# Kernel optimization log

Hardware: AMD Instinct MI355X
Metric: run time of the kernel (lower is better)

The kernel has to match this reference:

```python
import jax, jax.numpy as jnp
import numpy as np

HEADS = 4
DIM_HEAD = 32
HIDDEN = HEADS * DIM_HEAD  # 128
SCALE = 10.0
EPS = 1e-12  # F.normalize eps


def _l2norm_lastdim(t):
    # F.normalize(t, dim=-1): t / max(||t||_2, eps) along last axis
    n = jnp.sqrt(jnp.sum(t * t, axis=-1, keepdims=True))
    return t / jnp.maximum(n, EPS)


def setup_inputs() -> dict:
    key = jax.random.key(0)
    k1, k2, k3 = jax.random.split(key, 3)
    x = jax.random.normal(k1, (2, 256, 4096), dtype=jnp.float32)
    w_qkv = jax.random.normal(k2, (3 * HIDDEN, 256), dtype=jnp.float32) * 0.05
    w_out = jax.random.normal(k3, (256, HIDDEN), dtype=jnp.float32) * 0.05
    b_out = jnp.zeros((256,), dtype=jnp.float32)
    return {"x": x, "w_qkv": w_qkv, "w_out": w_out, "b_out": b_out}


def reference(x, w_qkv, w_out, b_out):
    b, c, l = x.shape
    # pointwise Conv1d == channel matmul: (3*hidden, c) @ (b, c, l)
    qkv = jnp.einsum('oc,bcl->bol', w_qkv, x)
    q, k, v = jnp.split(qkv, 3, axis=1)
    resh = lambda t: t.reshape(b, HEADS, DIM_HEAD, l)  # (b,h,d,l)
    q, k, v = resh(q), resh(k), resh(v)
    # faithful: normalize over the LAST dim (sequence axis l)
    q = _l2norm_lastdim(q)
    k = _l2norm_lastdim(k)
    sim = jnp.einsum('bhdi,bhdj->bhij', q, k) * SCALE  # (b,h,l,l)
    attn = jax.nn.softmax(sim, axis=-1)
    out = jnp.einsum('bhij,bhdj->bhid', attn, v)  # (b,h,l,d)
    # faithful raw view: row-major reshape of (b,h,l,d) -> (b, h*d, l)
    out = out.reshape(b, HIDDEN, l)
    return jnp.einsum('oc,bcl->bol', w_out, out) + b_out[None, :, None]
```

## Files before the change

kernel.cpp:

```cpp
#include <hip/hip_runtime.h>
#include <math.h>

#define LSEQ 4096
#define CIN  256
#define HID  128
#define O3   384
#define NSP  4
#define JTPS (64 / NSP)

typedef float f32x4 __attribute__((ext_vector_type(4)));
typedef short s16x8 __attribute__((ext_vector_type(8)));
typedef short s16x4 __attribute__((ext_vector_type(4)));

typedef const __attribute__((address_space(1))) char* gp_t;
typedef __attribute__((address_space(3))) char* lp_t;

__device__ __forceinline__ short f2bf(float f) {
    union { float f; unsigned u; } c; c.f = f;
    unsigned r = (c.u + 0x7FFFu + ((c.u >> 16) & 1u)) >> 16;
    return (short)r;
}

__device__ __forceinline__ unsigned cvt_pk_bf16(float lo, float hi) {
    unsigned r;
    asm("v_cvt_pk_bf16_f32 %0, %1, %2" : "=v"(r) : "v"(lo), "v"(hi));
    return r;
}

__device__ __forceinline__ float exp2_hw(float x) {
    float r;
    asm("v_exp_f32 %0, %1" : "=v"(r) : "v"(x));
    return r;
}

__device__ __forceinline__ float bfbits(unsigned v, int hi) {
    union { unsigned u; float f; } c;
    c.u = hi ? (v & 0xffff0000u) : (v << 16);
    return c.f;
}

__global__ __launch_bounds__(256) void pack_xw(const float* __restrict__ x,
                                               const float* __restrict__ wq,
                                               const float* __restrict__ wo,
                                               short* __restrict__ xP,
                                               short* __restrict__ wP,
                                               short* __restrict__ wP2) {
    const int tid = threadIdx.x;
    if (blockIdx.x >= 1024) {
        const int gid = (blockIdx.x - 1024) * 256 + tid;
        s16x8 o;
        if (gid < 12288) {
            const int m = gid & 15, g = (gid >> 4) & 3, ct = (gid >> 6) & 7;
            const int ot = gid >> 9;
            const float* src = wq + (ot * 16 + m) * 256 + ct * 32 + g * 8;
#pragma unroll
            for (int e = 0; e < 8; ++e) o[e] = f2bf(src[e]);
            *(s16x8*)(wP + (size_t)gid * 8) = o;
        } else {
            const int g2 = gid - 12288;
            const int m = g2 & 15, g = (g2 >> 4) & 3, ct = (g2 >> 6) & 3;
            const int ot = g2 >> 8;
            const float* src = wo + (ot * 16 + m) * 128 + ct * 32 + g * 8;
#pragma unroll
            for (int e = 0; e < 8; ++e) o[e] = f2bf(src[e]);
            *(s16x8*)(wP2 + (size_t)g2 * 8) = o;
        }
        return;
    }
    __shared__ float tile[32][68];
    const int b = blockIdx.x >> 9, ct = (blockIdx.x >> 6) & 7, lt = blockIdx.x & 63;
    const int c = tid >> 3, l8 = (tid & 7) * 8;
    const float* xb = x + ((size_t)b * CIN + ct * 32 + c) * LSEQ + lt * 64 + l8;
    *(float4*)&tile[c][l8]     = *(const float4*)xb;
    *(float4*)&tile[c][l8 + 4] = *(const float4*)(xb + 4);
    __syncthreads();
    const int g = tid >> 6, l = tid & 63;
    s16x8 o;
#pragma unroll
    for (int e = 0; e < 8; ++e) o[e] = f2bf(tile[g * 8 + e][l]);
    *(s16x8*)(xP + ((size_t)((b * 8 + ct) * 4 + g) * LSEQ + lt * 64 + l) * 8) = o;
}

__global__ __launch_bounds__(256) void mfma_qkv(const short* __restrict__ xP,
                                                const short* __restrict__ wP,
                                                float* __restrict__ qkv) {
    const int i = blockIdx.x;
    const int slice = i & 31, ot = i >> 5;
    const int b = slice >> 4, lq = slice & 15;
    const int tid = threadIdx.x, lane = tid & 63, w = tid >> 6;
    const int m = lane & 15, g = lane >> 4;
    const int l0 = lq * 256 + w * 64;

    s16x8 wA[8];
#pragma unroll
    for (int ct = 0; ct < 8; ++ct)
        wA[ct] = *(const s16x8*)(wP + ((size_t)((ot * 8 + ct) * 4 + g) * 16 + m) * 8);

    f32x4 acc[4];
#pragma unroll
    for (int t = 0; t < 4; ++t) acc[t] = (f32x4){0.f, 0.f, 0.f, 0.f};

#pragma unroll
    for (int ct = 0; ct < 8; ++ct) {
        const size_t bb = (size_t)((b * 8 + ct) * 4 + g) * LSEQ;
#pragma unroll
        for (int t = 0; t < 4; ++t) {
            const s16x8 xf = *(const s16x8*)(xP + (bb + l0 + t * 16 + m) * 8);
            acc[t] = __builtin_amdgcn_mfma_f32_16x16x32_bf16(wA[ct], xf, acc[t], 0, 0, 0);
        }
    }
    float* qb = qkv + ((size_t)b * O3 + ot * 16) * LSEQ;
#pragma unroll
    for (int t = 0; t < 4; ++t)
#pragma unroll
        for (int r = 0; r < 4; ++r)
            qb[(size_t)(4 * g + r) * LSEQ + l0 + t * 16 + m] = acc[t][r];
}

__global__ __launch_bounds__(256) void k_norm(const float* __restrict__ qkv,
                                              float* __restrict__ scales) {
    const int row = blockIdx.x;
    const int b = row >> 8, o = row & 255;
    const float* p = qkv + ((size_t)b * O3 + o) * LSEQ;
    const int tid = threadIdx.x;
    float ss = 0.f;
#pragma unroll
    for (int r = 0; r < 4; ++r) {
        const float4 v = *(const float4*)(p + (r * 256 + tid) * 4);
        ss += v.x * v.x + v.y * v.y + v.z * v.z + v.w * v.w;
    }
#pragma unroll
    for (int off = 32; off >= 1; off >>= 1) ss += __shfl_xor(ss, off);
    __shared__ float red[4];
    if ((tid & 63) == 0) red[tid >> 6] = ss;
    __syncthreads();
    if (tid == 0) {
        const float tot = red[0] + red[1] + red[2] + red[3];
        const float num = (o < HID) ? 14.4269504088896340736f : 1.0f;
        scales[row] = num / fmaxf(sqrtf(tot), 1e-12f);
    }
}

__global__ __launch_bounds__(256) void k_pack(const float* __restrict__ qkv,
                                              const float* __restrict__ scales,
                                              short* __restrict__ qT,
                                              short* __restrict__ kP,
                                              short* __restrict__ vP) {
    __shared__ float tile[32][68];
    const int tid = threadIdx.x;
    const int bh = blockIdx.x & 7, ch = blockIdx.x >> 3;
    const int b = bh >> 2, h = bh & 3;
    const int l0 = ch * 64;
    const float* qg = qkv + ((size_t)b * O3 + h * 32) * LSEQ;
    const float* kg = qg + (size_t)HID * LSEQ;
    const float* vg = qg + (size_t)2 * HID * LSEQ;
    const size_t bho = (size_t)bh * (LSEQ * 32);
    const int d = tid >> 3, c8 = (tid & 7) * 8;

    *(float4*)&tile[d][c8]     = *(const float4*)(qg + (size_t)d * LSEQ + l0 + c8);
    *(float4*)&tile[d][c8 + 4] = *(const float4*)(qg + (size_t)d * LSEQ + l0 + c8 + 4);
    __syncthreads();
    {
        const int i = tid >> 2, dseg = (tid & 3) * 8;
        const float4 sa = *(const float4*)(scales + b * 256 + h * 32 + dseg);
        const float4 sb = *(const float4*)(scales + b * 256 + h * 32 + dseg + 4);
        const float sc[8] = {sa.x, sa.y, sa.z, sa.w, sb.x, sb.y, sb.z, sb.w};
        s16x8 o;
#pragma unroll
        for (int e = 0; e < 8; ++e) o[e] = f2bf(tile[dseg + e][i] * sc[e]);
        *(s16x8*)(qT + bho + (size_t)(l0 + i) * 32 + dseg) = o;
    }
    __syncthreads();
    *(float4*)&tile[d][c8]     = *(const float4*)(kg + (size_t)d * LSEQ + l0 + c8);
    *(float4*)&tile[d][c8 + 4] = *(const float4*)(kg + (size_t)d * LSEQ + l0 + c8 + 4);
    __syncthreads();
    {
        const int gg = tid >> 6, jl = tid & 63;
        const float4 sa = *(const float4*)(scales + b * 256 + 128 + h * 32 + gg * 8);
        const float4 sb = *(const float4*)(scales + b * 256 + 128 + h * 32 + gg * 8 + 4);
        const float sc[8] = {sa.x, sa.y, sa.z, sa.w, sb.x, sb.y, sb.z, sb.w};
        s16x8 o;
#pragma unroll
        for (int e = 0; e < 8; ++e) o[e] = f2bf(tile[gg * 8 + e][jl] * sc[e]);
        *(s16x8*)(kP + bho + (size_t)ch * 2048 + gg * 512 + jl * 8) = o;
    }
    __syncthreads();
    *(float4*)&tile[d][c8]     = *(const float4*)(vg + (size_t)d * LSEQ + l0 + c8);
    *(float4*)&tile[d][c8 + 4] = *(const float4*)(vg + (size_t)d * LSEQ + l0 + c8 + 4);
    __syncthreads();
    {
        const int s = tid >> 4, dd = (tid & 15) * 2;
        s16x8 o;
#pragma unroll
        for (int u = 0; u < 4; ++u) {
            o[u]     = f2bf(tile[dd][s * 4 + u]);
            o[4 + u] = f2bf(tile[dd + 1][s * 4 + u]);
        }
        *(s16x8*)(vP + bho + (size_t)ch * 2048 + s * 128 + dd * 4) = o;
    }
}

__global__ __launch_bounds__(512, 8) void k_attn(const short* __restrict__ qT,
                                                 const short* __restrict__ kP,
                                                 const short* __restrict__ vP,
                                                 unsigned* __restrict__ pacc2,
                                                 float* __restrict__ plsum) {
    __shared__ float4 lds_v[1024];
    char* lds = (char*)lds_v;
    const int tid = threadIdx.x;
    const int lane = tid & 63, w = tid >> 6;
    const int m = lane & 15, g = lane >> 4;
    const int bh = blockIdx.x & 7;
    const int rest = blockIdx.x >> 3;
    const int iblk = rest & 31, sp = rest >> 5;
    const size_t bho = (size_t)bh * (LSEQ * 32);
    const int i0 = iblk * 128 + w * 16;

    const s16x8 qf = *(const s16x8*)(qT + bho + (size_t)(i0 + m) * 32 + g * 8);
    const char* kPb = (const char*)(kP + bho);
    const char* vPb = (const char*)(vP + bho);

    float lsum = 0.f;
    f32x4 acc0 = {0.f, 0.f, 0.f, 0.f}, acc1 = {0.f, 0.f, 0.f, 0.f};
    const f32x4 zeroc = {0.f, 0.f, 0.f, 0.f};
    const int jt0 = sp * JTPS;

    auto stage = [&](int buf, int jt) {
        const char* src = (tid < 256 ? kPb : vPb) + (size_t)jt * 4096 + (tid & 255) * 16;
        char* dst = lds + buf * 8192 + (tid < 256 ? 0 : 4096) + (w & 3) * 1024;
        __builtin_amdgcn_global_load_lds((gp_t)src, (lp_t)dst, 16, 0, 0);
    };

    stage(0, jt0);
    __syncthreads();

    for (int t = 0; t < JTPS; ++t) {
        const int buf = t & 1;
        if (t + 1 < JTPS) stage(buf ^ 1, jt0 + t + 1);
        const char* kb = lds + buf * 8192;
        const char* vb = kb + 4096;

        f32x4 st[4];
#pragma unroll
        for (int t2 = 0; t2 < 4; ++t2) {
            const s16x8 kf = *(const s16x8*)(kb + g * 1024 + (t2 * 16 + m) * 16);
            st[t2] = __builtin_amdgcn_mfma_f32_16x16x32_bf16(kf, qf, zeroc, 0, 0, 0);
        }

        float p[16];
        float ts0 = 0.f, ts1 = 0.f, ts2 = 0.f, ts3 = 0.f;
#pragma unroll
        for (int t2 = 0; t2 < 4; ++t2) {
            const float e0 = exp2_hw(st[t2][0]);
            const float e1 = exp2_hw(st[t2][1]);
            const float e2 = exp2_hw(st[t2][2]);
            const float e3 = exp2_hw(st[t2][3]);
            p[t2 * 4 + 0] = e0; p[t2 * 4 + 1] = e1;
            p[t2 * 4 + 2] = e2; p[t2 * 4 + 3] = e3;
            ts0 += e0; ts1 += e1; ts2 += e2; ts3 += e3;
        }
        lsum += (ts0 + ts1) + (ts2 + ts3);

        union { unsigned u[4]; s16x8 v; } a0u, a1u;
#pragma unroll
        for (int e = 0; e < 4; ++e) {
            a0u.u[e] = cvt_pk_bf16(p[2 * e],     p[2 * e + 1]);
            a1u.u[e] = cvt_pk_bf16(p[8 + 2 * e], p[9 + 2 * e]);
        }

#pragma unroll
        for (int pp = 0; pp < 2; ++pp) {
            const s16x8 pa = pp ? a1u.v : a0u.v;
#pragma unroll
            for (int n0 = 0; n0 < 2; ++n0) {
                const s16x4 v0 = *(const s16x4*)(vb + (pp * 8 + 0 + g) * 256 + (n0 * 16 + m) * 8);
                const s16x4 v1 = *(const s16x4*)(vb + (pp * 8 + 4 + g) * 256 + (n0 * 16 + m) * 8);
                s16x8 vf;
#pragma unroll
                for (int u = 0; u < 4; ++u) { vf[u] = v0[u]; vf[4 + u] = v1[u]; }
                if (n0 == 0) acc0 = __builtin_amdgcn_mfma_f32_16x16x32_bf16(pa, vf, acc0, 0, 0, 0);
                else         acc1 = __builtin_amdgcn_mfma_f32_16x16x32_bf16(pa, vf, acc1, 0, 0, 0);
            }
        }
        __syncthreads();
    }

    lsum += __shfl_xor(lsum, 16);
    lsum += __shfl_xor(lsum, 32);

    const int pb = (bh * 32 + iblk) * NSP + sp;
    if (g == 0) plsum[(size_t)pb * 128 + w * 16 + m] = lsum;
    unsigned* pa = pacc2 + ((size_t)pb * 128 + w * 16) * 16;
#pragma unroll
    for (int r = 0; r < 4; ++r)
        pa[(g * 4 + r) * 16 + m] = cvt_pk_bf16(acc0[r], acc1[r]);
}

__global__ __launch_bounds__(256) void k_comb(const unsigned* __restrict__ pacc2,
                                              const float* __restrict__ plsum,
                                              short* __restrict__ rawP) {
    const int b = blockIdx.x >> 6, lblk = blockIdx.x & 63;
    const int l0 = lblk * 64;
    const int t = threadIdx.x;
    const int ct2 = t >> 6, g = (t >> 4) & 3, lsub = t & 15;
    const int ii = (l0 + lsub * 4) >> 5;
    const int mm0 = (lsub * 4) & 15;
    const int hi = (lsub >> 2) & 1;

#pragma unroll
    for (int e = 0; e < 8; ++e) {
        const int row0 = (((b * 4 + ct2) * 32) + g * 8 + e) * NSP;
        float ls = 0.f, a0 = 0.f, a1 = 0.f, a2 = 0.f, a3 = 0.f;
#pragma unroll
        for (int sp = 0; sp < NSP; ++sp) {
            const unsigned* pr = pacc2 + ((size_t)(row0 + sp) * 128 + ii) * 16 + mm0;
            const uint4 u = *(const uint4*)pr;
            a0 += bfbits(u.x, hi); a1 += bfbits(u.y, hi);
            a2 += bfbits(u.z, hi); a3 += bfbits(u.w, hi);
            ls += plsum[(size_t)(row0 + sp) * 128 + ii];
        }
        const float inv = 1.0f / ls;
        short* dst = rawP + (((size_t)((b * 4 + ct2) * 4 + g) * LSEQ) + l0 + lsub * 4) * 8 + e;
        dst[0]  = f2bf(a0 * inv);
        dst[8]  = f2bf(a1 * inv);
        dst[16] = f2bf(a2 * inv);
        dst[24] = f2bf(a3 * inv);
    }
}

__global__ __launch_bounds__(256) void mfma_proj(const short* __restrict__ rawP,
                                                 const short* __restrict__ wP2,
                                                 const float* __restrict__ bias,
                                                 float* __restrict__ out) {
    const int i = blockIdx.x;
    const int slice = i & 31, ot = i >> 5;
    const int b = slice >> 4, lq = slice & 15;
    const int tid = threadIdx.x, lane = tid & 63, w = tid >> 6;
    const int m = lane & 15, g = lane >> 4;
    const int l0 = lq * 256 + w * 64;

    s16x8 wA[4];
#pragma unroll
    for (int ct = 0; ct < 4; ++ct)
        wA[ct] = *(const s16x8*)(wP2 + ((size_t)((ot * 4 + ct) * 4 + g) * 16 + m) * 8);

    f32x4 acc[4];
#pragma unroll
    for (int t = 0; t < 4; ++t) acc[t] = (f32x4){0.f, 0.f, 0.f, 0.f};

#pragma unroll
    for (int ct = 0; ct < 4; ++ct) {
        const size_t bb = (size_t)((b * 4 + ct) * 4 + g) * LSEQ;
#pragma unroll
        for (int t = 0; t < 4; ++t) {
            const s16x8 xf = *(const s16x8*)(rawP + (bb + l0 + t * 16 + m) * 8);
            acc[t] = __builtin_amdgcn_mfma_f32_16x16x32_bf16(wA[ct], xf, acc[t], 0, 0, 0);
        }
    }
    float bv[4];
#pragma unroll
    for (int r = 0; r < 4; ++r) bv[r] = bias[ot * 16 + 4 * g + r];
    float* ob = out + ((size_t)b * CIN + ot * 16) * LSEQ;
#pragma unroll
    for (int t = 0; t < 4; ++t)
#pragma unroll
        for (int r = 0; r < 4; ++r)
            ob[(size_t)(4 * g + r) * LSEQ + l0 + t * 16 + m] = acc[t][r] + bv[r];
}

extern "C" void kernel_launch(void* const* d_in, const int* in_sizes, int n_in,
                              void* d_out, int out_size, void* d_ws, size_t ws_size,
                              hipStream_t stream) {
    const float* x     = (const float*)d_in[0];
    const float* w_qkv = (const float*)d_in[1];
    const float* w_out = (const float*)d_in[2];
    const float* b_out = (const float*)d_in[3];
    float* out = (float*)d_out;
    float* ws  = (float*)d_ws;

    float*    qkv    = ws;
    unsigned* pacc2  = (unsigned*)ws;
    short*    rawP   = (short*)(ws + 2097152);
    float*    plsum  = ws + 2621440;
    short*    xP     = (short*)(ws + 3145728);
    short*    qT     = (short*)(ws + 3145728);
    short*    kP     = (short*)(ws + 3670016);
    short*    vP     = (short*)(ws + 4194304);
    short*    wP     = (short*)(ws + 4718592);
    short*    wP2    = (short*)(ws + 4767744);
    float*    scales = ws + 4784128;

    pack_xw  <<<1088, 256, 0, stream>>>(x, w_qkv, w_out, xP, wP, wP2);
    mfma_qkv <<<768,  256, 0, stream>>>(xP, wP, qkv);
    k_norm   <<<512,  256, 0, stream>>>(qkv, scales);
    k_pack   <<<512,  256, 0, stream>>>(qkv, scales, qT, kP, vP);
    k_attn   <<<1024, 512, 0, stream>>>(qT, kP, vP, pacc2, plsum);
    k_comb   <<<128,  256, 0, stream>>>(pacc2, plsum, rawP);
    mfma_proj<<<512,  256, 0, stream>>>(rawP, wP2, b_out, out);
}
```

Baseline: 72.74 us.

## Fuse L2-norm reduction into QKV GEMM, store QKV as bf16, repack V

After: 67.17 us. 7.7% less time.

```diff
diff --git a/kernel.cpp b/kernel.cpp
--- a/kernel.cpp
+++ b/kernel.cpp
@@ -21,6 +21,12 @@
     return (short)r;
 }
 
+__device__ __forceinline__ float bf2f(short s) {
+    union { unsigned u; float f; } c;
+    c.u = ((unsigned)(unsigned short)s) << 16;
+    return c.f;
+}
+
 __device__ __forceinline__ unsigned cvt_pk_bf16(float lo, float hi) {
     unsigned r;
     asm("v_cvt_pk_bf16_f32 %0, %1, %2" : "=v"(r) : "v"(lo), "v"(hi));
@@ -44,9 +50,11 @@
                                                const float* __restrict__ wo,
                                                short* __restrict__ xP,
                                                short* __restrict__ wP,
-                                               short* __restrict__ wP2) {
+                                               short* __restrict__ wP2,
+                                               float* __restrict__ ss) {
     const int tid = threadIdx.x;
     if (blockIdx.x >= 1024) {
+        if (blockIdx.x == 1024) { ss[tid] = 0.f; ss[256 + tid] = 0.f; }
         const int gid = (blockIdx.x - 1024) * 256 + tid;
         s16x8 o;
         if (gid < 12288) {
@@ -83,7 +91,8 @@
 
 __global__ __launch_bounds__(256) void mfma_qkv(const short* __restrict__ xP,
                                                 const short* __restrict__ wP,
-                                                float* __restrict__ qkv) {
+                                                short* __restrict__ qkv,
+                                                float* __restrict__ ss) {
     const int i = blockIdx.x;
     const int slice = i & 31, ot = i >> 5;
     const int b = slice >> 4, lq = slice & 15;
@@ -109,40 +118,34 @@
             acc[t] = __builtin_amdgcn_mfma_f32_16x16x32_bf16(wA[ct], xf, acc[t], 0, 0, 0);
         }
     }
-    float* qb = qkv + ((size_t)b * O3 + ot * 16) * LSEQ;
+    short* qb = qkv + ((size_t)b * O3 + ot * 16) * LSEQ;
 #pragma unroll
     for (int t = 0; t < 4; ++t)
 #pragma unroll
         for (int r = 0; r < 4; ++r)
-            qb[(size_t)(4 * g + r) * LSEQ + l0 + t * 16 + m] = acc[t][r];
-}
-
-__global__ __launch_bounds__(256) void k_norm(const float* __restrict__ qkv,
-                                              float* __restrict__ scales) {
-    const int row = blockIdx.x;
-    const int b = row >> 8, o = row & 255;
-    const float* p = qkv + ((size_t)b * O3 + o) * LSEQ;
-    const int tid = threadIdx.x;
-    float ss = 0.f;
-#pragma unroll
-    for (int r = 0; r < 4; ++r) {
-        const float4 v = *(const float4*)(p + (r * 256 + tid) * 4);
-        ss += v.x * v.x + v.y * v.y + v.z * v.z + v.w * v.w;
-    }
-#pragma unroll
-    for (int off = 32; off >= 1; off >>= 1) ss += __shfl_xor(ss, off);
-    __shared__ float red[4];
-    if ((tid & 63) == 0) red[tid >> 6] = ss;
-    __syncthreads();
-    if (tid == 0) {
-        const float tot = red[0] + red[1] + red[2] + red[3];
-        const float num = (o < HID) ? 14.4269504088896340736f : 1.0f;
-        scales[row] = num / fmaxf(sqrtf(tot), 1e-12f);
-    }
-}
-
-__global__ __launch_bounds__(256) void k_pack(const float* __restrict__ qkv,
-                                              const float* __restrict__ scales,
+            qb[(size_t)(4 * g + r) * LSEQ + l0 + t * 16 + m] = f2bf(acc[t][r]);
+
+    if (ot < 16) {
+        float s4[4];
+#pragma unroll
+        for (int r = 0; r < 4; ++r) {
+            float s = acc[0][r] * acc[0][r];
+#pragma unroll
+            for (int t = 1; t < 4; ++t) s = fmaf(acc[t][r], acc[t][r], s);
+#pragma unroll
+            for (int mk = 1; mk < 16; mk <<= 1) s += __shfl_xor(s, mk);
+            s4[r] = s;
+        }
+        if (m == 0) {
+#pragma unroll
+            for (int r = 0; r < 4; ++r)
+                atomicAdd(ss + b * 256 + ot * 16 + 4 * g + r, s4[r]);
+        }
+    }
+}
+
+__global__ __launch_bounds__(256) void k_pack(const short* __restrict__ qkv,
+                                              const float* __restrict__ ss,
                                               short* __restrict__ qT,
                                               short* __restrict__ kP,
                                               short* __restrict__ vP) {
@@ -151,52 +154,61 @@
     const int bh = blockIdx.x & 7, ch = blockIdx.x >> 3;
     const int b = bh >> 2, h = bh & 3;
     const int l0 = ch * 64;
-    const float* qg = qkv + ((size_t)b * O3 + h * 32) * LSEQ;
-    const float* kg = qg + (size_t)HID * LSEQ;
-    const float* vg = qg + (size_t)2 * HID * LSEQ;
+    const short* qg = qkv + ((size_t)b * O3 + h * 32) * LSEQ;
+    const short* kg = qg + (size_t)HID * LSEQ;
+    const short* vg = qg + (size_t)2 * HID * LSEQ;
     const size_t bho = (size_t)bh * (LSEQ * 32);
     const int d = tid >> 3, c8 = (tid & 7) * 8;
 
-    *(float4*)&tile[d][c8]     = *(const float4*)(qg + (size_t)d * LSEQ + l0 + c8);
-    *(float4*)&tile[d][c8 + 4] = *(const float4*)(qg + (size_t)d * LSEQ + l0 + c8 + 4);
+    {
+        const s16x8 qv = *(const s16x8*)(qg + (size_t)d * LSEQ + l0 + c8);
+#pragma unroll
+        for (int e = 0; e < 8; ++e) tile[d][c8 + e] = bf2f(qv[e]);
+    }
     __syncthreads();
     {
         const int i = tid >> 2, dseg = (tid & 3) * 8;
-        const float4 sa = *(const float4*)(scales + b * 256 + h * 32 + dseg);
-        const float4 sb = *(const float4*)(scales + b * 256 + h * 32 + dseg + 4);
-        const float sc[8] = {sa.x, sa.y, sa.z, sa.w, sb.x, sb.y, sb.z, sb.w};
         s16x8 o;
 #pragma unroll
-        for (int e = 0; e < 8; ++e) o[e] = f2bf(tile[dseg + e][i] * sc[e]);
+        for (int e = 0; e < 8; ++e) {
+            const float sc = 14.4269504088896340736f /
+                             fmaxf(sqrtf(ss[b * 256 + h * 32 + dseg + e]), 1e-12f);
+            o[e] = f2bf(tile[dseg + e][i] * sc);
+        }
         *(s16x8*)(qT + bho + (size_t)(l0 + i) * 32 + dseg) = o;
     }
     __syncthreads();
-    *(float4*)&tile[d][c8]     = *(const float4*)(kg + (size_t)d * LSEQ + l0 + c8);
-    *(float4*)&tile[d][c8 + 4] = *(const float4*)(kg + (size_t)d * LSEQ + l0 + c8 + 4);
+    {
+        const s16x8 kv = *(const s16x8*)(kg + (size_t)d * LSEQ + l0 + c8);
+#pragma unroll
+        for (int e = 0; e < 8; ++e) tile[d][c8 + e] = bf2f(kv[e]);
+    }
     __syncthreads();
     {
         const int gg = tid >> 6, jl = tid & 63;
-        const float4 sa = *(const float4*)(scales + b * 256 + 128 + h * 32 + gg * 8);
-        const float4 sb = *(const float4*)(scales + b * 256 + 128 + h * 32 + gg * 8 + 4);
-        const float sc[8] = {sa.x, sa.y, sa.z, sa.w, sb.x, sb.y, sb.z, sb.w};
         s16x8 o;
 #pragma unroll
-        for (int e = 0; e < 8; ++e) o[e] = f2bf(tile[gg * 8 + e][jl] * sc[e]);
+        for (int e = 0; e < 8; ++e) {
+            const float sc = 1.0f /
+                             fmaxf(sqrtf(ss[b * 256 + 128 + h * 32 + gg * 8 + e]), 1e-12f);
+            o[e] = f2bf(tile[gg * 8 + e][jl] * sc);
+        }
         *(s16x8*)(kP + bho + (size_t)ch * 2048 + gg * 512 + jl * 8) = o;
     }
     __syncthreads();
-    *(float4*)&tile[d][c8]     = *(const float4*)(vg + (size_t)d * LSEQ + l0 + c8);
-    *(float4*)&tile[d][c8 + 4] = *(const float4*)(vg + (size_t)d * LSEQ + l0 + c8 + 4);
-    __syncthreads();
-    {
-        const int s = tid >> 4, dd = (tid & 15) * 2;
+    {
+        const s16x8 vv = *(const s16x8*)(vg + (size_t)d * LSEQ + l0 + c8);
+#pragma unroll
+        for (int e = 0; e < 8; ++e) tile[d][c8 + e] = bf2f(vv[e]);
+    }
+    __syncthreads();
+    {
+        const int pp = tid >> 7, g = (tid >> 5) & 3, dd = tid & 31;
         s16x8 o;
 #pragma unroll
-        for (int u = 0; u < 4; ++u) {
-            o[u]     = f2bf(tile[dd][s * 4 + u]);
-            o[4 + u] = f2bf(tile[dd + 1][s * 4 + u]);
-        }
-        *(s16x8*)(vP + bho + (size_t)ch * 2048 + s * 128 + dd * 4) = o;
+        for (int e = 0; e < 8; ++e)
+            o[e] = f2bf(tile[dd][pp * 32 + ((e >> 2) * 16) + g * 4 + (e & 3)]);
+        *(s16x8*)(vP + bho + (size_t)ch * 2048 + tid * 8) = o;
     }
 }
 
@@ -273,11 +285,7 @@
             const s16x8 pa = pp ? a1u.v : a0u.v;
 #pragma unroll
             for (int n0 = 0; n0 < 2; ++n0) {
-                const s16x4 v0 = *(const s16x4*)(vb + (pp * 8 + 0 + g) * 256 + (n0 * 16 + m) * 8);
-                const s16x4 v1 = *(const s16x4*)(vb + (pp * 8 + 4 + g) * 256 + (n0 * 16 + m) * 8);
-                s16x8 vf;
-#pragma unroll
-                for (int u = 0; u < 4; ++u) { vf[u] = v0[u]; vf[4 + u] = v1[u]; }
+                const s16x8 vf = *(const s16x8*)(vb + (pp * 128 + g * 32 + n0 * 16 + m) * 16);
                 if (n0 == 0) acc0 = __builtin_amdgcn_mfma_f32_16x16x32_bf16(pa, vf, acc0, 0, 0, 0);
                 else         acc1 = __builtin_amdgcn_mfma_f32_16x16x32_bf16(pa, vf, acc1, 0, 0, 0);
             }
@@ -378,22 +386,21 @@
     float* out = (float*)d_out;
     float* ws  = (float*)d_ws;
 
-    float*    qkv    = ws;
+    short*    qkv    = (short*)ws;
     unsigned* pacc2  = (unsigned*)ws;
     short*    rawP   = (short*)(ws + 2097152);
     float*    plsum  = ws + 2621440;
-    short*    xP     = (short*)(ws + 3145728);
-    short*    qT     = (short*)(ws + 3145728);
-    short*    kP     = (short*)(ws + 3670016);
-    short*    vP     = (short*)(ws + 4194304);
-    short*    wP     = (short*)(ws + 4718592);
-    short*    wP2    = (short*)(ws + 4767744);
-    float*    scales = ws + 4784128;
-
-    pack_xw  <<<1088, 256, 0, stream>>>(x, w_qkv, w_out, xP, wP, wP2);
-    mfma_qkv <<<768,  256, 0, stream>>>(xP, wP, qkv);
-    k_norm   <<<512,  256, 0, stream>>>(qkv, scales);
-    k_pack   <<<512,  256, 0, stream>>>(qkv, scales, qT, kP, vP);
+    short*    xP     = (short*)(ws + 2752512);
+    short*    qT     = (short*)(ws + 2752512);
+    short*    kP     = (short*)(ws + 3276800);
+    short*    vP     = (short*)(ws + 3801088);
+    short*    wP     = (short*)(ws + 4325376);
+    short*    wP2    = (short*)(ws + 4374528);
+    float*    ss     = ws + 4390912;
+
+    pack_xw  <<<1088, 256, 0, stream>>>(x, w_qkv, w_out, xP, wP, wP2, ss);
+    mfma_qkv <<<768,  256, 0, stream>>>(xP, wP, qkv, ss);
+    k_pack   <<<512,  256, 0, stream>>>(qkv, ss, qT, kP, vP);
     k_attn   <<<1024, 512, 0, stream>>>(qT, kP, vP, pacc2, plsum);
     k_comb   <<<128,  256, 0, stream>>>(pacc2, plsum, rawP);
     mfma_proj<<<512,  256, 0, stream>>>(rawP, wP2, b_out, out);
```
